# Kernel optimization log

Hardware: AMD Instinct MI355X
Metric: run time of the kernel (lower is better)

## Reference

```python
import jax, jax.numpy as jnp
import numpy as np

NUM_HEADS = 16


def setup_inputs() -> dict:
    key = jax.random.key(0)
    ks = jax.random.split(key, 5)
    B, S, D = 4, 2048, 1024
    scale = 1.0 / np.sqrt(D)
    return {
        "x": jax.random.normal(ks[0], (B, S, D), dtype=jnp.float32),
        "Wq": jax.random.normal(ks[1], (D, D), dtype=jnp.float32) * scale,
        "Wk": jax.random.normal(ks[2], (D, D), dtype=jnp.float32) * scale,
        "Wv": jax.random.normal(ks[3], (D, D), dtype=jnp.float32) * scale,
        "Wo": jax.random.normal(ks[4], (D, D), dtype=jnp.float32) * scale,
    }


def reference(x, Wq, Wk, Wv, Wo):
    # x: [B, S, D]; weights are torch Linear weights [out, in], applied as x @ W.T
    B, S, D = x.shape
    H = NUM_HEADS
    dk = D // H

    def split_heads(t):  # [B,S,D] -> [B,H,S,dk]
        return t.reshape(B, S, H, dk).transpose(0, 2, 1, 3)

    q = split_heads(x @ Wq.T)
    k = split_heads(x @ Wk.T)
    v = split_heads(x @ Wv.T)

    scores = jnp.einsum("bhqd,bhkd->bhqk", q, k) / jnp.sqrt(jnp.float32(dk))
    causal = jnp.triu(jnp.ones((S, S), dtype=bool), k=1)  # True above diagonal
    scores = jnp.where(causal, -jnp.inf, scores)
    probs = jax.nn.softmax(scores, axis=-1)

    out = jnp.einsum("bhqk,bhkd->bhqd", probs, v)  # [B,H,S,dk]
    out = out.transpose(0, 2, 1, 3).reshape(B, S, D)
    return out @ Wo.T
```

## Files before the change

kernel.cpp:

```cpp
#include <hip/hip_runtime.h>

typedef __bf16 bf16_t;
using bf16x8 = __attribute__((ext_vector_type(8))) __bf16;
using bf16x4 = __attribute__((ext_vector_type(4))) __bf16;
using f32x4  = __attribute__((ext_vector_type(4))) float;

#define B_   4
#define S_   2048
#define D_   1024
#define H_   16
#define DK_  64
#define SQKV 3072

__device__ __forceinline__ void gload_lds16(const void* g, void* l) {
  __builtin_amdgcn_global_load_lds((const __attribute__((address_space(1))) void*)g,
                                   (__attribute__((address_space(3))) void*)l, 16, 0, 0);
}

__device__ __forceinline__ float fast_exp2(float x) {
#if __has_builtin(__builtin_amdgcn_exp2f)
  return __builtin_amdgcn_exp2f(x);
#else
  return __expf(x * 0.69314718f);
#endif
}

__global__ void cast_f32_to_bf16(const float* __restrict__ in, bf16_t* __restrict__ out,
                                 int n4, float scale) {
  int i = blockIdx.x * 256 + threadIdx.x;
  if (i >= n4) return;
  float4 v = reinterpret_cast<const float4*>(in)[i];
  bf16x4 o;
  o[0] = (bf16_t)(v.x * scale); o[1] = (bf16_t)(v.y * scale);
  o[2] = (bf16_t)(v.z * scale); o[3] = (bf16_t)(v.w * scale);
  reinterpret_cast<bf16x4*>(out)[i] = o;
}

template <typename OutT>
__global__ void gemm_bt(const bf16_t* __restrict__ A, const bf16_t* __restrict__ Bm,
                        OutT* __restrict__ C, int M, int N, int K) {
  __shared__ alignas(16) char As[16384];
  __shared__ alignas(16) char Bs[16384];
  const int tid  = threadIdx.x;
  const int wid  = tid >> 6, lane = tid & 63;
  const int g    = lane >> 4, l15 = lane & 15;

  int nwg = gridDim.x * gridDim.y;
  int bid = blockIdx.y * gridDim.x + blockIdx.x;
  int sb  = ((nwg & 7) == 0) ? ((bid & 7) * (nwg >> 3) + (bid >> 3)) : bid;
  int bx  = sb % gridDim.x, by = sb / gridDim.x;

  const long row0 = (long)by * 128, col0 = (long)bx * 128;
  const int wr = (wid >> 1) * 64, wc = (wid & 1) * 64;
  f32x4 acc[4][4] = {};

  for (int k0 = 0; k0 < K; k0 += 64) {
    __syncthreads();
#pragma unroll
    for (int i = 0; i < 4; ++i) {
      int L = i * 256 + tid;
      int r = L >> 3, s = L & 7;
      int sc = s ^ (r & 7);
      const bf16_t* ga = A  + (row0 + r) * (long)K + k0 + sc * 8;
      const bf16_t* gb = Bm + (col0 + r) * (long)K + k0 + sc * 8;
      gload_lds16(ga, As + (i * 256 + wid * 64) * 16);
      gload_lds16(gb, Bs + (i * 256 + wid * 64) * 16);
    }
    __syncthreads();
#pragma unroll
    for (int kk = 0; kk < 2; ++kk) {
      bf16x8 af[4], bfr[4];
#pragma unroll
      for (int m = 0; m < 4; ++m) {
        int r = wr + m * 16 + l15;
        int s = (kk * 4 + g) ^ (r & 7);
        af[m] = *reinterpret_cast<const bf16x8*>(As + r * 128 + s * 16);
      }
#pragma unroll
      for (int n = 0; n < 4; ++n) {
        int r = wc + n * 16 + l15;
        int s = (kk * 4 + g) ^ (r & 7);
        bfr[n] = *reinterpret_cast<const bf16x8*>(Bs + r * 128 + s * 16);
      }
#pragma unroll
      for (int m = 0; m < 4; ++m)
#pragma unroll
        for (int n = 0; n < 4; ++n)
          acc[m][n] = __builtin_amdgcn_mfma_f32_16x16x32_bf16(af[m], bfr[n], acc[m][n], 0, 0, 0);
    }
  }
#pragma unroll
  for (int m = 0; m < 4; ++m)
#pragma unroll
    for (int n = 0; n < 4; ++n)
#pragma unroll
      for (int j = 0; j < 4; ++j) {
        long r = row0 + wr + m * 16 + g * 4 + j;
        long c = col0 + wc + n * 16 + l15;
        C[r * (long)N + c] = (OutT)acc[m][n][j];
      }
}

__global__ void vtrans_kernel(const bf16_t* __restrict__ qkv, bf16_t* __restrict__ VT) {
  __shared__ bf16_t t[64 * 65];
  const int tid = threadIdx.x;
  const int s0 = blockIdx.x * 64;
  const int bh = blockIdx.y, b = bh >> 4, h = bh & 15;
  {
    int sl = tid >> 2, dc = tid & 3;
    const bf16_t* src = qkv + ((long)(b * S_ + s0 + sl)) * SQKV + 2 * D_ + h * DK_ + dc * 16;
    bf16x8 v0 = *reinterpret_cast<const bf16x8*>(src);
    bf16x8 v1 = *reinterpret_cast<const bf16x8*>(src + 8);
#pragma unroll
    for (int e = 0; e < 8; ++e) t[sl * 65 + dc * 16 + e] = v0[e];
#pragma unroll
    for (int e = 0; e < 8; ++e) t[sl * 65 + dc * 16 + 8 + e] = v1[e];
  }
  __syncthreads();
  {
    int d = tid >> 2, sc = tid & 3;
    bf16x8 o0, o1;
#pragma unroll
    for (int e = 0; e < 8; ++e) o0[e] = t[(sc * 16 + e) * 65 + d];
#pragma unroll
    for (int e = 0; e < 8; ++e) o1[e] = t[(sc * 16 + 8 + e) * 65 + d];
    bf16_t* dst = VT + ((long)(bh * 64 + d)) * S_ + s0 + sc * 16;
    *reinterpret_cast<bf16x8*>(dst) = o0;
    *reinterpret_cast<bf16x8*>(dst + 8) = o1;
  }
}

__global__ __launch_bounds__(256, 4)
void attn_kernel(const bf16_t* __restrict__ qkv, const bf16_t* __restrict__ VT,
                 bf16_t* __restrict__ Ob) {
  __shared__ alignas(16) char ldsK[2][8192];
  __shared__ alignas(16) char ldsV[2][8192];
  __shared__ alignas(16) char ldsP[4][2048];
  const int tid = threadIdx.x;
  const int w   = tid >> 6, lane = tid & 63;
  const int g   = lane >> 4, l15 = lane & 15;

  int bid = blockIdx.y * 32 + blockIdx.x;
  int sb  = (bid & 7) * 256 + (bid >> 3);
  const int qt = 31 - (sb & 31);
  const int bh = sb >> 5;
  const int b  = bh >> 4, h = bh & 15;
  const long rowbase = (long)b * S_;

  bf16x8 qf[2];
  {
    const bf16_t* qp = qkv + (rowbase + qt * 64 + w * 16 + l15) * SQKV + h * DK_ + g * 8;
    qf[0] = *reinterpret_cast<const bf16x8*>(qp);
    qf[1] = *reinterpret_cast<const bf16x8*>(qp + 32);
  }
  float m_j[4], ssum[4] = {0.f, 0.f, 0.f, 0.f};
#pragma unroll
  for (int j = 0; j < 4; ++j) m_j[j] = -1e30f;
  f32x4 oacc[4] = {};

  const bf16_t* kbase = qkv + rowbase * SQKV + D_ + h * DK_;
  const bf16_t* vbase = VT + (long)bh * 64 * S_;

  auto stageK = [&](int kvt, int buf) {
#pragma unroll
    for (int i = 0; i < 2; ++i) {
      int L = i * 256 + tid;
      int r = L >> 3, s = L & 7;
      int sc = s ^ (r & 7);
      gload_lds16(kbase + (long)(kvt * 64 + r) * SQKV + sc * 8,
                  ldsK[buf] + L * 16);
    }
  };
  auto stageV = [&](int kvt, int buf) {
#pragma unroll
    for (int i = 0; i < 2; ++i) {
      int L = i * 256 + tid;
      int r = L >> 3, s = L & 7;
      int sc = s ^ (r & 7);
      gload_lds16(vbase + (long)r * S_ + kvt * 64 + sc * 8,
                  ldsV[buf] + L * 16);
    }
  };

  stageK(0, 0); stageV(0, 0);

  for (int kvt = 0; kvt <= qt; ++kvt) {
    const int cur = kvt & 1;
    asm volatile("s_waitcnt vmcnt(0)" ::: "memory");
    __builtin_amdgcn_s_barrier();
    if (kvt < qt) { stageK(kvt + 1, cur ^ 1); stageV(kvt + 1, cur ^ 1); }

    f32x4 sv[4];
    __builtin_amdgcn_s_setprio(1);
#pragma unroll
    for (int c = 0; c < 4; ++c) {
      f32x4 a = {};
#pragma unroll
      for (int kk = 0; kk < 2; ++kk) {
        int r = c * 16 + l15;
        int s = (kk * 4 + g) ^ (l15 & 7);
        bf16x8 kf = *reinterpret_cast<const bf16x8*>(ldsK[cur] + r * 128 + s * 16);
        a = __builtin_amdgcn_mfma_f32_16x16x32_bf16(qf[kk], kf, a, 0, 0, 0);
      }
      sv[c] = a;
    }
    __builtin_amdgcn_s_setprio(0);

    if (kvt == qt) {
#pragma unroll
      for (int j = 0; j < 4; ++j) {
        int ql = w * 16 + g * 4 + j;
#pragma unroll
        for (int c = 0; c < 4; ++c)
          if ((c * 16 + l15) > ql) sv[c][j] = -1e30f;
      }
    }

    float mx[4];
#pragma unroll
    for (int j = 0; j < 4; ++j)
      mx[j] = fmaxf(fmaxf(sv[0][j], sv[1][j]), fmaxf(sv[2][j], sv[3][j]));
    bool need = false;
#pragma unroll
    for (int j = 0; j < 4; ++j) need |= (mx[j] > m_j[j] + 8.0f);
    if (__any(need)) {
#pragma unroll
      for (int off = 1; off < 16; off <<= 1)
#pragma unroll
        for (int j = 0; j < 4; ++j) mx[j] = fmaxf(mx[j], __shfl_xor(mx[j], off));
#pragma unroll
      for (int j = 0; j < 4; ++j) {
        float mn = fmaxf(m_j[j], mx[j]);
        float al = fast_exp2(m_j[j] - mn);
        m_j[j] = mn;
        ssum[j] *= al;
#pragma unroll
        for (int dc = 0; dc < 4; ++dc) oacc[dc][j] *= al;
      }
    }

    bf16_t* pw = (bf16_t*)ldsP[w];
#pragma unroll
    for (int c = 0; c < 4; ++c)
#pragma unroll
      for (int j = 0; j < 4; ++j) {
        float p = fast_exp2(sv[c][j] - m_j[j]);
        ssum[j] += p;
        int q = g * 4 + j;
        int chunk = (c * 2 + (l15 >> 3)) ^ (q & 7);
        pw[q * 64 + chunk * 8 + (l15 & 7)] = (bf16_t)p;
      }

    __builtin_amdgcn_s_setprio(1);
#pragma unroll
    for (int ks = 0; ks < 2; ++ks) {
      int sp = (ks * 4 + g) ^ (l15 & 7);
      bf16x8 pf = *reinterpret_cast<const bf16x8*>(ldsP[w] + l15 * 128 + sp * 16);
#pragma unroll
      for (int dc = 0; dc < 4; ++dc) {
        int r = dc * 16 + l15;
        int s = (ks * 4 + g) ^ (l15 & 7);
        bf16x8 vf = *reinterpret_cast<const bf16x8*>(ldsV[cur] + r * 128 + s * 16);
        oacc[dc] = __builtin_amdgcn_mfma_f32_16x16x32_bf16(pf, vf, oacc[dc], 0, 0, 0);
      }
    }
    __builtin_amdgcn_s_setprio(0);
  }

#pragma unroll
  for (int off = 1; off < 16; off <<= 1)
#pragma unroll
    for (int j = 0; j < 4; ++j) ssum[j] += __shfl_xor(ssum[j], off);
#pragma unroll
  for (int j = 0; j < 4; ++j) {
    float inv = 1.0f / ssum[j];
    long r = rowbase + qt * 64 + w * 16 + g * 4 + j;
#pragma unroll
    for (int dc = 0; dc < 4; ++dc)
      Ob[r * D_ + h * DK_ + dc * 16 + l15] = (bf16_t)(oacc[dc][j] * inv);
  }
}

extern "C" void kernel_launch(void* const* d_in, const int* in_sizes, int n_in,
                              void* d_out, int out_size, void* d_ws, size_t ws_size,
                              hipStream_t stream) {
  const float* x  = (const float*)d_in[0];
  const float* Wq = (const float*)d_in[1];
  const float* Wk = (const float*)d_in[2];
  const float* Wv = (const float*)d_in[3];
  const float* Wo = (const float*)d_in[4];
  float* out = (float*)d_out;

  char* ws = (char*)d_ws;
  bf16_t* xb  = (bf16_t*)(ws);
  bf16_t* Wc  = (bf16_t*)(ws + 16777216);
  bf16_t* Wob = (bf16_t*)(ws + 23068672);
  bf16_t* QKV = (bf16_t*)(ws + 25165824);
  bf16_t* Ob  = (bf16_t*)(ws + 75497472);
  bf16_t* VT  = xb;

  const float QSCALE = 0.18033688f;

  cast_f32_to_bf16<<<8192, 256, 0, stream>>>(x,  xb,            2097152, 1.0f);
  cast_f32_to_bf16<<<1024, 256, 0, stream>>>(Wq, Wc,             262144, QSCALE);
  cast_f32_to_bf16<<<1024, 256, 0, stream>>>(Wk, Wc + 1048576,   262144, 1.0f);
  cast_f32_to_bf16<<<1024, 256, 0, stream>>>(Wv, Wc + 2097152,   262144, 1.0f);
  cast_f32_to_bf16<<<1024, 256, 0, stream>>>(Wo, Wob,            262144, 1.0f);

  gemm_bt<bf16_t><<<dim3(24, 64), 256, 0, stream>>>(xb, Wc, QKV, 8192, 3072, 1024);
  vtrans_kernel<<<dim3(32, 64), 256, 0, stream>>>(QKV, VT);
  attn_kernel<<<dim3(32, 64), 256, 0, stream>>>(QKV, VT, Ob);
  gemm_bt<float><<<dim3(8, 64), 256, 0, stream>>>(Ob, Wob, out, 8192, 1024, 1024);
}
```

Measured before the change: 281.3 us.

## Compute transposed S to keep P in registers and drop the LDS round trip

Swaps the MFMA operand order so each lane holds scores for a single query row, which lets the P fragment feed the PV MFMA straight from registers. The per-warp LDS staging buffer for P is removed. To make this work, the V transpose kernel writes its key positions in a permuted order that matches the register layout of P. Row max and sum reductions shrink to two cross-lane shuffles, the output store becomes a 4-wide vector, and the occupancy hint rises to 5 blocks per SIMD, which trades fewer available registers for more resident waves.

```diff
diff --git a/kernel.cpp b/kernel.cpp
--- a/kernel.cpp
+++ b/kernel.cpp
@@ -121,21 +121,28 @@
     int d = tid >> 2, sc = tid & 3;
     bf16x8 o0, o1;
 #pragma unroll
-    for (int e = 0; e < 8; ++e) o0[e] = t[(sc * 16 + e) * 65 + d];
-#pragma unroll
-    for (int e = 0; e < 8; ++e) o1[e] = t[(sc * 16 + 8 + e) * 65 + d];
+    for (int e = 0; e < 8; ++e) {
+      int p  = sc * 16 + e;
+      int kv = ((p >> 5) << 5) + (((p >> 2) & 1) << 4) + (((p >> 3) & 3) << 2) + (p & 3);
+      o0[e] = t[kv * 65 + d];
+    }
+#pragma unroll
+    for (int e = 0; e < 8; ++e) {
+      int p  = sc * 16 + 8 + e;
+      int kv = ((p >> 5) << 5) + (((p >> 2) & 1) << 4) + (((p >> 3) & 3) << 2) + (p & 3);
+      o1[e] = t[kv * 65 + d];
+    }
     bf16_t* dst = VT + ((long)(bh * 64 + d)) * S_ + s0 + sc * 16;
     *reinterpret_cast<bf16x8*>(dst) = o0;
     *reinterpret_cast<bf16x8*>(dst + 8) = o1;
   }
 }
 
-__global__ __launch_bounds__(256, 4)
+__global__ __launch_bounds__(256, 5)
 void attn_kernel(const bf16_t* __restrict__ qkv, const bf16_t* __restrict__ VT,
                  bf16_t* __restrict__ Ob) {
   __shared__ alignas(16) char ldsK[2][8192];
   __shared__ alignas(16) char ldsV[2][8192];
-  __shared__ alignas(16) char ldsP[4][2048];
   const int tid = threadIdx.x;
   const int w   = tid >> 6, lane = tid & 63;
   const int g   = lane >> 4, l15 = lane & 15;
@@ -153,9 +160,7 @@
     qf[0] = *reinterpret_cast<const bf16x8*>(qp);
     qf[1] = *reinterpret_cast<const bf16x8*>(qp + 32);
   }
-  float m_j[4], ssum[4] = {0.f, 0.f, 0.f, 0.f};
-#pragma unroll
-  for (int j = 0; j < 4; ++j) m_j[j] = -1e30f;
+  float m_q = -1e30f, ssum = 0.f;
   f32x4 oacc[4] = {};
 
   const bf16_t* kbase = qkv + rowbase * SQKV + D_ + h * DK_;
@@ -184,6 +189,9 @@
 
   stageK(0, 0); stageV(0, 0);
 
+  const int ql = w * 16 + l15;
+  const int gj = g * 4;
+
   for (int kvt = 0; kvt <= qt; ++kvt) {
     const int cur = kvt & 1;
     asm volatile("s_waitcnt vmcnt(0)" ::: "memory");
@@ -200,7 +208,7 @@
         int r = c * 16 + l15;
         int s = (kk * 4 + g) ^ (l15 & 7);
         bf16x8 kf = *reinterpret_cast<const bf16x8*>(ldsK[cur] + r * 128 + s * 16);
-        a = __builtin_amdgcn_mfma_f32_16x16x32_bf16(qf[kk], kf, a, 0, 0, 0);
+        a = __builtin_amdgcn_mfma_f32_16x16x32_bf16(kf, qf[kk], a, 0, 0, 0);
       }
       sv[c] = a;
     }
@@ -208,76 +216,67 @@
 
     if (kvt == qt) {
 #pragma unroll
-      for (int j = 0; j < 4; ++j) {
-        int ql = w * 16 + g * 4 + j;
-#pragma unroll
-        for (int c = 0; c < 4; ++c)
-          if ((c * 16 + l15) > ql) sv[c][j] = -1e30f;
-      }
-    }
-
-    float mx[4];
-#pragma unroll
-    for (int j = 0; j < 4; ++j)
-      mx[j] = fmaxf(fmaxf(sv[0][j], sv[1][j]), fmaxf(sv[2][j], sv[3][j]));
-    bool need = false;
-#pragma unroll
-    for (int j = 0; j < 4; ++j) need |= (mx[j] > m_j[j] + 8.0f);
-    if (__any(need)) {
-#pragma unroll
-      for (int off = 1; off < 16; off <<= 1)
-#pragma unroll
-        for (int j = 0; j < 4; ++j) mx[j] = fmaxf(mx[j], __shfl_xor(mx[j], off));
-#pragma unroll
-      for (int j = 0; j < 4; ++j) {
-        float mn = fmaxf(m_j[j], mx[j]);
-        float al = fast_exp2(m_j[j] - mn);
-        m_j[j] = mn;
-        ssum[j] *= al;
-#pragma unroll
-        for (int dc = 0; dc < 4; ++dc) oacc[dc][j] *= al;
-      }
-    }
-
-    bf16_t* pw = (bf16_t*)ldsP[w];
+      for (int c = 0; c < 4; ++c)
+#pragma unroll
+        for (int j = 0; j < 4; ++j)
+          if ((c * 16 + gj + j) > ql) sv[c][j] = -1e30f;
+    }
+
+    float mxi = sv[0][0];
 #pragma unroll
     for (int c = 0; c < 4; ++c)
 #pragma unroll
-      for (int j = 0; j < 4; ++j) {
-        float p = fast_exp2(sv[c][j] - m_j[j]);
-        ssum[j] += p;
-        int q = g * 4 + j;
-        int chunk = (c * 2 + (l15 >> 3)) ^ (q & 7);
-        pw[q * 64 + chunk * 8 + (l15 & 7)] = (bf16_t)p;
+      for (int j = 0; j < 4; ++j) mxi = fmaxf(mxi, sv[c][j]);
+    if (__any(mxi > m_q + 8.0f)) {
+      float mx = fmaxf(mxi, __shfl_xor(mxi, 16));
+      mx = fmaxf(mx, __shfl_xor(mx, 32));
+      float mn = fmaxf(m_q, mx);
+      float al = fast_exp2(m_q - mn);
+      m_q = mn;
+      ssum *= al;
+#pragma unroll
+      for (int dc = 0; dc < 4; ++dc)
+#pragma unroll
+        for (int j = 0; j < 4; ++j) oacc[dc][j] *= al;
+    }
+
+    bf16x8 pb[2];
+#pragma unroll
+    for (int ks = 0; ks < 2; ++ks)
+#pragma unroll
+      for (int half = 0; half < 2; ++half) {
+        int c = ks * 2 + half;
+#pragma unroll
+        for (int j = 0; j < 4; ++j) {
+          float p = fast_exp2(sv[c][j] - m_q);
+          ssum += p;
+          pb[ks][half * 4 + j] = (bf16_t)p;
+        }
       }
 
     __builtin_amdgcn_s_setprio(1);
 #pragma unroll
-    for (int ks = 0; ks < 2; ++ks) {
-      int sp = (ks * 4 + g) ^ (l15 & 7);
-      bf16x8 pf = *reinterpret_cast<const bf16x8*>(ldsP[w] + l15 * 128 + sp * 16);
+    for (int ks = 0; ks < 2; ++ks)
 #pragma unroll
       for (int dc = 0; dc < 4; ++dc) {
         int r = dc * 16 + l15;
         int s = (ks * 4 + g) ^ (l15 & 7);
         bf16x8 vf = *reinterpret_cast<const bf16x8*>(ldsV[cur] + r * 128 + s * 16);
-        oacc[dc] = __builtin_amdgcn_mfma_f32_16x16x32_bf16(pf, vf, oacc[dc], 0, 0, 0);
-      }
-    }
+        oacc[dc] = __builtin_amdgcn_mfma_f32_16x16x32_bf16(vf, pb[ks], oacc[dc], 0, 0, 0);
+      }
     __builtin_amdgcn_s_setprio(0);
   }
 
-#pragma unroll
-  for (int off = 1; off < 16; off <<= 1)
-#pragma unroll
-    for (int j = 0; j < 4; ++j) ssum[j] += __shfl_xor(ssum[j], off);
-#pragma unroll
-  for (int j = 0; j < 4; ++j) {
-    float inv = 1.0f / ssum[j];
-    long r = rowbase + qt * 64 + w * 16 + g * 4 + j;
-#pragma unroll
-    for (int dc = 0; dc < 4; ++dc)
-      Ob[r * D_ + h * DK_ + dc * 16 + l15] = (bf16_t)(oacc[dc][j] * inv);
+  ssum += __shfl_xor(ssum, 16);
+  ssum += __shfl_xor(ssum, 32);
+  float inv = 1.0f / ssum;
+  long r = rowbase + qt * 64 + w * 16 + l15;
+#pragma unroll
+  for (int dc = 0; dc < 4; ++dc) {
+    bf16x4 o;
+#pragma unroll
+    for (int j = 0; j < 4; ++j) o[j] = (bf16_t)(oacc[dc][j] * inv);
+    *reinterpret_cast<bf16x4*>(&Ob[r * D_ + h * DK_ + dc * 16 + gj]) = o;
   }
 }
 
```

Result: faster. 254.8 us (-9.4%).
